# Kernel tuning notes

Hardware: AMD Instinct MI355X
Metric: run time of the kernel (lower is better)

The kernel has to match this reference:

```python
import jax, jax.numpy as jnp
import numpy as np

IN_FEA = 128
OUT_FEA = 128
ALPHA = 0.2  # LeakyReLU negative slope
NEG_INF = -1.0e12


def setup_inputs() -> dict:
    key = jax.random.key(0)
    k1, k2, k3, k4 = jax.random.split(key, 4)
    b, n = 8, 2048
    inp = jax.random.normal(k1, (b, n, IN_FEA), dtype=jnp.float32)
    adj = jax.random.randint(k2, (b, n, n), 0, 2, dtype=jnp.int32)
    # xavier_uniform with gain=1.414
    def xavier(k, shape, gain=1.414):
        fan_in, fan_out = shape[0], shape[1]
        limit = gain * np.sqrt(6.0 / (fan_in + fan_out))
        return jax.random.uniform(k, shape, jnp.float32, -limit, limit)
    W = xavier(k3, (IN_FEA, OUT_FEA))
    a = xavier(k4, (2 * OUT_FEA, 1))
    return {"inp": inp, "adj": adj, "W": W, "a": a}


def reference(inp, adj, W, a):
    # h: [b, n, d]
    h = jnp.matmul(inp, W)
    # Original builds [b, n*n, 2d] via repeat/view; equivalently split a into
    # a1 (applied to h_j, the 'chunks' half) and a2 (applied to h_i).
    d = h.shape[-1]
    a1 = a[:d, 0]   # [d]
    a2 = a[d:, 0]   # [d]
    f1 = jnp.einsum('bnd,d->bn', h, a1)  # contributes per-column (j)
    f2 = jnp.einsum('bnd,d->bn', h, a2)  # contributes per-row (i)
    e = jax.nn.leaky_relu(f2[:, :, None] + f1[:, None, :], negative_slope=ALPHA)  # [b, n, n]
    logits = jnp.where(adj > 0, e, NEG_INF)
    attention = jax.nn.softmax(logits, axis=-1)
    out_h = jnp.matmul(attention, h)
    out_h = jax.nn.elu(out_h) + h  # concat=True branch
    return out_h
```

## Files before the change

kernel.cpp:

```cpp
#include <hip/hip_runtime.h>
#include <hip/hip_bf16.h>

typedef __bf16 bf16x8 __attribute__((ext_vector_type(8)));
typedef __bf16 bf16x4 __attribute__((ext_vector_type(4)));
typedef float  f32x4  __attribute__((ext_vector_type(4)));

#define LRELU_ALPHA 0.2f
#define LOG2E 1.44269504088896340736f

__device__ __forceinline__ float fexp2(float x) {
#if __has_builtin(__builtin_amdgcn_exp2f)
    return __builtin_amdgcn_exp2f(x);
#else
    float r; asm("v_exp_f32 %0, %1" : "=v"(r) : "v"(x)); return r;
#endif
}

__device__ __forceinline__ void wg_barrier() {
    asm volatile("s_waitcnt lgkmcnt(0)" ::: "memory");
    __builtin_amdgcn_s_barrier();
    asm volatile("" ::: "memory");
}

__global__ __launch_bounds__(128) void gat_prep(
    const float* __restrict__ inp, const float* __restrict__ W,
    const float* __restrict__ a,
    __bf16* __restrict__ hb, float* __restrict__ f1, float* __restrict__ f2)
{
    const int r0 = blockIdx.x << 3;
    const int d  = threadIdx.x;
    __shared__ float sIn[8][128];
    __shared__ float sRed[8][4];
    #pragma unroll
    for (int r = 0; r < 8; ++r)
        sIn[r][d] = inp[(size_t)(r0 + r) * 128 + d];
    __syncthreads();

    float acc[8] = {0.f,0.f,0.f,0.f,0.f,0.f,0.f,0.f};
    #pragma unroll 4
    for (int k = 0; k < 128; ++k) {
        float wv = W[k * 128 + d];
        #pragma unroll
        for (int r = 0; r < 8; ++r) acc[r] += sIn[r][k] * wv;
    }

    const float a1 = a[d], a2 = a[128 + d];
    const int wv = d >> 6;
    #pragma unroll
    for (int r = 0; r < 8; ++r) {
        hb[(size_t)(r0 + r) * 128 + d] = (__bf16)acc[r];
        float t1 = acc[r] * a1;
        float t2 = acc[r] * a2;
        #pragma unroll
        for (int m = 1; m < 64; m <<= 1) {
            t1 += __shfl_xor(t1, m);
            t2 += __shfl_xor(t2, m);
        }
        if ((d & 63) == 0) { sRed[r][wv] = t1; sRed[r][2 + wv] = t2; }
    }
    __syncthreads();
    if (d < 8) {
        f1[r0 + d] = (sRed[d][0] + sRed[d][1]) * LOG2E;
        f2[r0 + d] = (sRed[d][2] + sRed[d][3]) * LOG2E;
    }
}

__global__ __launch_bounds__(256) void gat_f1max(
    const float* __restrict__ f1, float* __restrict__ f1max)
{
    const int b = blockIdx.x;
    const int t = threadIdx.x;
    float m = -1e30f;
    for (int j = t; j < 2048; j += 256) m = fmaxf(m, f1[b * 2048 + j]);
    #pragma unroll
    for (int k = 1; k < 64; k <<= 1) m = fmaxf(m, __shfl_xor(m, k));
    __shared__ float sm[4];
    if ((t & 63) == 0) sm[t >> 6] = m;
    __syncthreads();
    if (t == 0) f1max[b] = fmaxf(fmaxf(sm[0], sm[1]), fmaxf(sm[2], sm[3]));
}

__global__ __launch_bounds__(256) void gat_pack(
    const __bf16* __restrict__ hb, __bf16* __restrict__ pack)
{
    __shared__ __bf16 tile[64][72];
    const int tid = threadIdx.x;
    const int bidx = blockIdx.x;
    const int b  = bidx >> 6;
    const int tI = bidx & 63;
    const int n0 = (tI >> 1) << 6;
    const int d0 = (tI & 1) << 6;
    #pragma unroll
    for (int pass = 0; pass < 2; ++pass) {
        int row = (tid >> 3) + (pass << 5);
        int c   = (tid & 7) << 3;
        *(bf16x8*)&tile[row][c] =
            *(const bf16x8*)(hb + (size_t)(b * 2048 + n0 + row) * 128 + d0 + c);
    }
    __syncthreads();
    const int lane = tid & 63;
    const int il = lane & 15;
    const int kg = lane >> 4;
    #pragma unroll
    for (int pass = 0; pass < 2; ++pass) {
        const int f  = (tid >> 6) + (pass << 2);
        const int Dl = f >> 1;
        const int jh = f & 1;
        union { __bf16 e[8]; bf16x8 v; } u;
        #pragma unroll
        for (int e = 0; e < 8; ++e)
            u.e[e] = tile[(jh << 5) + (kg << 3) + e][(Dl << 4) + il];
        const size_t off = (((size_t)(b << 5) + (n0 >> 6)) << 13)
                         + ((size_t)((((d0 >> 4) + Dl) << 1) | jh) << 9)
                         + (lane << 3);
        *(bf16x8*)(pack + off) = u.v;
    }
}

#define PCOMPUTE(TT, BUF) do {                                                \
    const int _jb = ((TT) << 6) + (pj4 << 2);                                 \
    float4 uu = *(const float4*)&us[_jb];                                     \
    float4 vv = *(const float4*)&vs[_jb];                                     \
    float p0 = (uu.x > ti) ? ai * uu.x : bi * vv.x;                           \
    float p1 = (uu.y > ti) ? ai * uu.y : bi * vv.y;                           \
    float p2 = (uu.z > ti) ? ai * uu.z : bi * vv.z;                           \
    float p3 = (uu.w > ti) ? ai * uu.w : bi * vv.w;                           \
    p0 = (gA.x > 0) ? p0 : 0.f;                                               \
    p1 = (gA.y > 0) ? p1 : 0.f;                                               \
    p2 = (gA.z > 0) ? p2 : 0.f;                                               \
    p3 = (gA.w > 0) ? p3 : 0.f;                                               \
    bf16x4 pb;                                                                \
    pb[0] = (__bf16)p0; pb[1] = (__bf16)p1;                                   \
    pb[2] = (__bf16)p2; pb[3] = (__bf16)p3;                                   \
    den += (float)pb[0] + (float)pb[1] + (float)pb[2] + (float)pb[3];         \
    *(bf16x4*)(&Ps[BUF][pwo]) = pb;                                           \
} while (0)

__global__ __launch_bounds__(512, 4) void gat_attn11(
    const int* __restrict__ adj, const __bf16* __restrict__ hb,
    const __bf16* __restrict__ pack, const float* __restrict__ f1g,
    const float* __restrict__ f2g, const float* __restrict__ f1maxg,
    float* __restrict__ out)
{
    const int bid = ((blockIdx.x & 7) << 6) | (blockIdx.x >> 3);
    const int b  = bid >> 6;
    const int i0 = (bid & 63) << 5;
    const int tid = threadIdx.x;

    __shared__ float us[2048];
    __shared__ float vs[2048];
    __shared__ alignas(16) __bf16 Ps[2][2048];
    __shared__ float lsum[32];

    {
        float4 fv = *(const float4*)&f1g[(b << 11) + (tid << 2)];
        float4 uu, vv;
        uu.x = fexp2(fv.x); uu.y = fexp2(fv.y);
        uu.z = fexp2(fv.z); uu.w = fexp2(fv.w);
        vv.x = fexp2(LRELU_ALPHA * fv.x); vv.y = fexp2(LRELU_ALPHA * fv.y);
        vv.z = fexp2(LRELU_ALPHA * fv.z); vv.w = fexp2(LRELU_ALPHA * fv.w);
        *(float4*)&us[tid << 2] = uu;
        *(float4*)&vs[tid << 2] = vv;
    }

    const int pi  = tid >> 4;
    const int pj4 = tid & 15;
    const float fm  = f1maxg[b];
    const float f2v = f2g[(b << 11) + i0 + pi];
    const float z   = f2v + fm;
    const float M   = fmaxf(z, LRELU_ALPHA * z);
    const float ai  = fexp2(f2v - M);
    const float bi  = fexp2(__builtin_fmaf(LRELU_ALPHA, f2v, -M));
    const float ti  = fexp2(-f2v);
    const int* ajp = adj + (((size_t)(b << 11) + i0 + pi) << 11) + (pj4 << 2);
    const int pwo = (pi << 6) + ((((pj4 << 3)) ^ ((pi & 7) << 4)) >> 1);

    const int w    = tid >> 6;
    const int lane = tid & 63;
    const int il   = lane & 15;
    const int kg   = lane >> 4;
    const int ig   = w & 1;
    const int dq   = w >> 1;
    const int ai2  = (ig << 4) + il;
    const int aof0 = (ai2 << 6) + (((kg << 4) ^ ((ai2 & 7) << 4)) >> 1);
    const int aof1 = (ai2 << 6) + (((64 | (kg << 4)) ^ ((ai2 & 7) << 4)) >> 1);
    const __bf16* pB = pack + (((size_t)b << 5) << 13) + (dq << 11) + (lane << 3);

    f32x4 acc0 = {0.f,0.f,0.f,0.f}, acc1 = {0.f,0.f,0.f,0.f};
    float den = 0.f;

    int4 gA  = *(const int4*)ajp;
    int4 gA2 = *(const int4*)(ajp + 64);
    bf16x8 Bc0 = *(const bf16x8*)(pB);
    bf16x8 Bc1 = *(const bf16x8*)(pB + 512);
    bf16x8 Bc2 = *(const bf16x8*)(pB + 1024);
    bf16x8 Bc3 = *(const bf16x8*)(pB + 1536);

    wg_barrier();

    PCOMPUTE(0, 0);
    gA = gA2;
    gA2 = *(const int4*)(ajp + 128);

    wg_barrier();

    for (int t = 0; t < 31; ++t) {
        const __bf16* pBn = pB + ((size_t)(t + 1) << 13);
        bf16x8 Bn0 = *(const bf16x8*)(pBn);
        bf16x8 Bn1 = *(const bf16x8*)(pBn + 512);
        bf16x8 Bn2 = *(const bf16x8*)(pBn + 1024);
        bf16x8 Bn3 = *(const bf16x8*)(pBn + 1536);

        bf16x8 A0 = *(const bf16x8*)(&Ps[t & 1][aof0]);
        bf16x8 A1 = *(const bf16x8*)(&Ps[t & 1][aof1]);

        PCOMPUTE(t + 1, (t + 1) & 1);
        gA = gA2;
        gA2 = *(const int4*)(ajp + (((t + 3) & 31) << 6));

        acc0 = __builtin_amdgcn_mfma_f32_16x16x32_bf16(A0, Bc0, acc0, 0, 0, 0);
        acc0 = __builtin_amdgcn_mfma_f32_16x16x32_bf16(A1, Bc1, acc0, 0, 0, 0);
        acc1 = __builtin_amdgcn_mfma_f32_16x16x32_bf16(A0, Bc2, acc1, 0, 0, 0);
        acc1 = __builtin_amdgcn_mfma_f32_16x16x32_bf16(A1, Bc3, acc1, 0, 0, 0);

        Bc0 = Bn0; Bc1 = Bn1; Bc2 = Bn2; Bc3 = Bn3;

        wg_barrier();
    }

    {
        bf16x8 A0 = *(const bf16x8*)(&Ps[1][aof0]);
        bf16x8 A1 = *(const bf16x8*)(&Ps[1][aof1]);
        acc0 = __builtin_amdgcn_mfma_f32_16x16x32_bf16(A0, Bc0, acc0, 0, 0, 0);
        acc0 = __builtin_amdgcn_mfma_f32_16x16x32_bf16(A1, Bc1, acc0, 0, 0, 0);
        acc1 = __builtin_amdgcn_mfma_f32_16x16x32_bf16(A0, Bc2, acc1, 0, 0, 0);
        acc1 = __builtin_amdgcn_mfma_f32_16x16x32_bf16(A1, Bc3, acc1, 0, 0, 0);
    }

    den += __shfl_xor(den, 1);
    den += __shfl_xor(den, 2);
    den += __shfl_xor(den, 4);
    den += __shfl_xor(den, 8);
    if (pj4 == 0) lsum[pi] = den;
    wg_barrier();

    #pragma unroll
    for (int r = 0; r < 4; ++r) {
        const int   row = (kg << 2) + r;
        const float dn  = lsum[(ig << 4) + row];
        const size_t gbase = (((size_t)(b << 11) + i0 + (ig << 4) + row) << 7)
                             + (dq << 5) + il;
        float v, e;
        v = acc0[r] / dn; e = (v > 0.f) ? v : (__expf(v) - 1.f);
        out[gbase] = e + (float)hb[gbase];
        v = acc1[r] / dn; e = (v > 0.f) ? v : (__expf(v) - 1.f);
        out[gbase + 16] = e + (float)hb[gbase + 16];
    }
}

extern "C" void kernel_launch(void* const* d_in, const int* in_sizes, int n_in,
                              void* d_out, int out_size, void* d_ws, size_t ws_size,
                              hipStream_t stream)
{
    const float* inp = (const float*)d_in[0];
    const int*   adj = (const int*)d_in[1];
    const float* W   = (const float*)d_in[2];
    const float* a   = (const float*)d_in[3];
    float* out = (float*)d_out;

    char* ws = (char*)d_ws;
    __bf16* hb    = (__bf16*)ws;
    __bf16* pack  = (__bf16*)(ws + (4 << 20));
    float*  f1    = (float*)(ws + (8 << 20));
    float*  f2    = (float*)(ws + (8 << 20) + 65536);
    float*  f1max = (float*)(ws + (8 << 20) + 131072);

    gat_prep<<<2048, 128, 0, stream>>>(inp, W, a, hb, f1, f2);
    gat_f1max<<<8, 256, 0, stream>>>(f1, f1max);
    gat_pack<<<512, 256, 0, stream>>>(hb, pack);
    gat_attn11<<<512, 512, 0, stream>>>(adj, hb, pack, f1, f2, f1max, out);
}
```

Measured before the change: 58.68 us.

## Restructure attention kernel to 16-row tiles with MFMA-computed softmax denominators

```diff
diff --git a/kernel.cpp b/kernel.cpp
--- a/kernel.cpp
+++ b/kernel.cpp
@@ -2,7 +2,6 @@
 #include <hip/hip_bf16.h>
 
 typedef __bf16 bf16x8 __attribute__((ext_vector_type(8)));
-typedef __bf16 bf16x4 __attribute__((ext_vector_type(4)));
 typedef float  f32x4  __attribute__((ext_vector_type(4)));
 
 #define LRELU_ALPHA 0.2f
@@ -117,143 +116,159 @@
     }
 }
 
-#define PCOMPUTE(TT, BUF) do {                                                \
-    const int _jb = ((TT) << 6) + (pj4 << 2);                                 \
-    float4 uu = *(const float4*)&us[_jb];                                     \
-    float4 vv = *(const float4*)&vs[_jb];                                     \
-    float p0 = (uu.x > ti) ? ai * uu.x : bi * vv.x;                           \
-    float p1 = (uu.y > ti) ? ai * uu.y : bi * vv.y;                           \
-    float p2 = (uu.z > ti) ? ai * uu.z : bi * vv.z;                           \
-    float p3 = (uu.w > ti) ? ai * uu.w : bi * vv.w;                           \
-    p0 = (gA.x > 0) ? p0 : 0.f;                                               \
-    p1 = (gA.y > 0) ? p1 : 0.f;                                               \
-    p2 = (gA.z > 0) ? p2 : 0.f;                                               \
-    p3 = (gA.w > 0) ? p3 : 0.f;                                               \
-    bf16x4 pb;                                                                \
-    pb[0] = (__bf16)p0; pb[1] = (__bf16)p1;                                   \
-    pb[2] = (__bf16)p2; pb[3] = (__bf16)p3;                                   \
-    den += (float)pb[0] + (float)pb[1] + (float)pb[2] + (float)pb[3];         \
-    *(bf16x4*)(&Ps[BUF][pwo]) = pb;                                           \
-} while (0)
-
-__global__ __launch_bounds__(512, 4) void gat_attn11(
+__global__ __launch_bounds__(256, 4) void gat_attn12(
     const int* __restrict__ adj, const __bf16* __restrict__ hb,
     const __bf16* __restrict__ pack, const float* __restrict__ f1g,
     const float* __restrict__ f2g, const float* __restrict__ f1maxg,
     float* __restrict__ out)
 {
-    const int bid = ((blockIdx.x & 7) << 6) | (blockIdx.x >> 3);
-    const int b  = bid >> 6;
-    const int i0 = (bid & 63) << 5;
+    const int bid = ((blockIdx.x & 7) << 7) | (blockIdx.x >> 3);
+    const int b  = bid >> 7;
+    const int i0 = (bid & 127) << 4;
     const int tid = threadIdx.x;
 
     __shared__ float us[2048];
     __shared__ float vs[2048];
-    __shared__ alignas(16) __bf16 Ps[2][2048];
-    __shared__ float lsum[32];
-
-    {
-        float4 fv = *(const float4*)&f1g[(b << 11) + (tid << 2)];
-        float4 uu, vv;
-        uu.x = fexp2(fv.x); uu.y = fexp2(fv.y);
-        uu.z = fexp2(fv.z); uu.w = fexp2(fv.w);
-        vv.x = fexp2(LRELU_ALPHA * fv.x); vv.y = fexp2(LRELU_ALPHA * fv.y);
-        vv.z = fexp2(LRELU_ALPHA * fv.z); vv.w = fexp2(LRELU_ALPHA * fv.w);
-        *(float4*)&us[tid << 2] = uu;
-        *(float4*)&vs[tid << 2] = vv;
-    }
+    __shared__ alignas(16) __bf16 Ps[2][16 * 136];
+    __shared__ float lsum[16];
 
     const int pi  = tid >> 4;
     const int pj4 = tid & 15;
+
+    const int* ajp  = adj + (((size_t)(b << 11) + i0 + pi) << 11) + (pj4 << 3);
+    const int* ajp8 = ajp + 1024;
+
     const float fm  = f1maxg[b];
     const float f2v = f2g[(b << 11) + i0 + pi];
-    const float z   = f2v + fm;
-    const float M   = fmaxf(z, LRELU_ALPHA * z);
-    const float ai  = fexp2(f2v - M);
-    const float bi  = fexp2(__builtin_fmaf(LRELU_ALPHA, f2v, -M));
-    const float ti  = fexp2(-f2v);
-    const int* ajp = adj + (((size_t)(b << 11) + i0 + pi) << 11) + (pj4 << 2);
-    const int pwo = (pi << 6) + ((((pj4 << 3)) ^ ((pi & 7) << 4)) >> 1);
+    const float zM  = f2v + fm;
+    const float M   = fmaxf(zM, LRELU_ALPHA * zM);
+    const float ai_ = fexp2(f2v - M);
+    const float bi_ = fexp2(__builtin_fmaf(LRELU_ALPHA, f2v, -M));
+
+    int4 As[3][2];
+    As[0][0] = *(const int4*)(ajp);        As[0][1] = *(const int4*)(ajp + 4);
+    As[1][0] = *(const int4*)(ajp + 128);  As[1][1] = *(const int4*)(ajp + 132);
+    As[2][0] = *(const int4*)(ajp + 256);  As[2][1] = *(const int4*)(ajp + 260);
+
+    {
+        const int jb = tid << 3;
+        float4 f0 = *(const float4*)&f1g[(b << 11) + jb];
+        float4 f1v = *(const float4*)&f1g[(b << 11) + jb + 4];
+        float4 uu0, uu1, vv0, vv1;
+        uu0.x = fexp2(f0.x);  uu0.y = fexp2(f0.y);
+        uu0.z = fexp2(f0.z);  uu0.w = fexp2(f0.w);
+        uu1.x = fexp2(f1v.x); uu1.y = fexp2(f1v.y);
+        uu1.z = fexp2(f1v.z); uu1.w = fexp2(f1v.w);
+        vv0.x = fexp2(LRELU_ALPHA * f0.x);  vv0.y = fexp2(LRELU_ALPHA * f0.y);
+        vv0.z = fexp2(LRELU_ALPHA * f0.z);  vv0.w = fexp2(LRELU_ALPHA * f0.w);
+        vv1.x = fexp2(LRELU_ALPHA * f1v.x); vv1.y = fexp2(LRELU_ALPHA * f1v.y);
+        vv1.z = fexp2(LRELU_ALPHA * f1v.z); vv1.w = fexp2(LRELU_ALPHA * f1v.w);
+        *(float4*)&us[jb]     = uu0;  *(float4*)&us[jb + 4] = uu1;
+        *(float4*)&vs[jb]     = vv0;  *(float4*)&vs[jb + 4] = vv1;
+    }
 
     const int w    = tid >> 6;
     const int lane = tid & 63;
     const int il   = lane & 15;
     const int kg   = lane >> 4;
-    const int ig   = w & 1;
-    const int dq   = w >> 1;
-    const int ai2  = (ig << 4) + il;
-    const int aof0 = (ai2 << 6) + (((kg << 4) ^ ((ai2 & 7) << 4)) >> 1);
-    const int aof1 = (ai2 << 6) + (((64 | (kg << 4)) ^ ((ai2 & 7) << 4)) >> 1);
-    const __bf16* pB = pack + (((size_t)b << 5) << 13) + (dq << 11) + (lane << 3);
-
-    f32x4 acc0 = {0.f,0.f,0.f,0.f}, acc1 = {0.f,0.f,0.f,0.f};
-    float den = 0.f;
-
-    int4 gA  = *(const int4*)ajp;
-    int4 gA2 = *(const int4*)(ajp + 64);
-    bf16x8 Bc0 = *(const bf16x8*)(pB);
-    bf16x8 Bc1 = *(const bf16x8*)(pB + 512);
-    bf16x8 Bc2 = *(const bf16x8*)(pB + 1024);
-    bf16x8 Bc3 = *(const bf16x8*)(pB + 1536);
+    const int dq   = w;
+
+    f32x4 acc0 = {0,0,0,0}, acc1 = {0,0,0,0}, accd = {0,0,0,0};
+    union { __bf16 e[8]; bf16x8 v; } ones;
+    #pragma unroll
+    for (int x = 0; x < 8; ++x) ones.e[x] = (__bf16)1.0f;
+    const bf16x8 onesv = ones.v;
+
+#define PCOMP(TT, BUF) do {                                                   \
+    const int _jb = ((TT) << 7) + (pj4 << 3);                                 \
+    float4 _u0 = *(const float4*)&us[_jb];                                    \
+    float4 _u1 = *(const float4*)&us[_jb + 4];                                \
+    float4 _v0 = *(const float4*)&vs[_jb];                                    \
+    float4 _v1 = *(const float4*)&vs[_jb + 4];                                \
+    int4 _aA = As[(TT) % 3][0];                                               \
+    int4 _aB = As[(TT) % 3][1];                                               \
+    union { __bf16 e[8]; bf16x8 v; } _pb;                                     \
+    _pb.e[0] = (__bf16)((_aA.x > 0) ? fmaxf(ai_ * _u0.x, bi_ * _v0.x) : 0.f); \
+    _pb.e[1] = (__bf16)((_aA.y > 0) ? fmaxf(ai_ * _u0.y, bi_ * _v0.y) : 0.f); \
+    _pb.e[2] = (__bf16)((_aA.z > 0) ? fmaxf(ai_ * _u0.z, bi_ * _v0.z) : 0.f); \
+    _pb.e[3] = (__bf16)((_aA.w > 0) ? fmaxf(ai_ * _u0.w, bi_ * _v0.w) : 0.f); \
+    _pb.e[4] = (__bf16)((_aB.x > 0) ? fmaxf(ai_ * _u1.x, bi_ * _v1.x) : 0.f); \
+    _pb.e[5] = (__bf16)((_aB.y > 0) ? fmaxf(ai_ * _u1.y, bi_ * _v1.y) : 0.f); \
+    _pb.e[6] = (__bf16)((_aB.z > 0) ? fmaxf(ai_ * _u1.z, bi_ * _v1.z) : 0.f); \
+    _pb.e[7] = (__bf16)((_aB.w > 0) ? fmaxf(ai_ * _u1.w, bi_ * _v1.w) : 0.f); \
+    *(bf16x8*)&Ps[BUF][pi * 136 + (pj4 << 3)] = _pb.v;                        \
+    if ((TT) + 3 < 16) {        \
+        if ((TT) + 3 < 8) {                                                   \
+            As[(TT) % 3][0] = *(const int4*)(ajp + (((TT) + 3) << 7));        \
+            As[(TT) % 3][1] = *(const int4*)(ajp + (((TT) + 3) << 7) + 4);    \
+        } else {                                                              \
+            As[(TT) % 3][0] = *(const int4*)(ajp8 + (((TT) - 5) << 7));       \
+            As[(TT) % 3][1] = *(const int4*)(ajp8 + (((TT) - 5) << 7) + 4);   \
+        }                                                                     \
+    }                                                                         \
+} while (0)
 
     wg_barrier();
-
-    PCOMPUTE(0, 0);
-    gA = gA2;
-    gA2 = *(const int4*)(ajp + 128);
-
+    PCOMP(0, 0);
     wg_barrier();
 
-    for (int t = 0; t < 31; ++t) {
-        const __bf16* pBn = pB + ((size_t)(t + 1) << 13);
-        bf16x8 Bn0 = *(const bf16x8*)(pBn);
-        bf16x8 Bn1 = *(const bf16x8*)(pBn + 512);
-        bf16x8 Bn2 = *(const bf16x8*)(pBn + 1024);
-        bf16x8 Bn3 = *(const bf16x8*)(pBn + 1536);
-
-        bf16x8 A0 = *(const bf16x8*)(&Ps[t & 1][aof0]);
-        bf16x8 A1 = *(const bf16x8*)(&Ps[t & 1][aof1]);
-
-        PCOMPUTE(t + 1, (t + 1) & 1);
-        gA = gA2;
-        gA2 = *(const int4*)(ajp + (((t + 3) & 31) << 6));
-
-        acc0 = __builtin_amdgcn_mfma_f32_16x16x32_bf16(A0, Bc0, acc0, 0, 0, 0);
-        acc0 = __builtin_amdgcn_mfma_f32_16x16x32_bf16(A1, Bc1, acc0, 0, 0, 0);
-        acc1 = __builtin_amdgcn_mfma_f32_16x16x32_bf16(A0, Bc2, acc1, 0, 0, 0);
-        acc1 = __builtin_amdgcn_mfma_f32_16x16x32_bf16(A1, Bc3, acc1, 0, 0, 0);
-
-        Bc0 = Bn0; Bc1 = Bn1; Bc2 = Bn2; Bc3 = Bn3;
+    #pragma unroll
+    for (int t = 0; t < 16; ++t) {
+        const __bf16* bp0 = pack + (((size_t)(b << 5) + (t << 1)) << 13)
+                          + (dq << 11) + (lane << 3);
+        const __bf16* bp1 = bp0 + 8192;
+        bf16x8 B00 = *(const bf16x8*)(bp0);
+        bf16x8 B01 = *(const bf16x8*)(bp0 + 512);
+        bf16x8 B02 = *(const bf16x8*)(bp0 + 1024);
+        bf16x8 B03 = *(const bf16x8*)(bp0 + 1536);
+        bf16x8 B10 = *(const bf16x8*)(bp1);
+        bf16x8 B11 = *(const bf16x8*)(bp1 + 512);
+        bf16x8 B12 = *(const bf16x8*)(bp1 + 1024);
+        bf16x8 B13 = *(const bf16x8*)(bp1 + 1536);
+
+        if (t < 15) PCOMP(t + 1, (t + 1) & 1);
+
+        const __bf16* pr = &Ps[t & 1][0];
+        const int abase = il * 136 + kg * 8;
+        bf16x8 Af0 = *(const bf16x8*)(pr + abase);
+        bf16x8 Af1 = *(const bf16x8*)(pr + abase + 32);
+        bf16x8 Af2 = *(const bf16x8*)(pr + abase + 64);
+        bf16x8 Af3 = *(const bf16x8*)(pr + abase + 96);
+
+        acc0 = __builtin_amdgcn_mfma_f32_16x16x32_bf16(Af0, B00, acc0, 0,0,0);
+        acc1 = __builtin_amdgcn_mfma_f32_16x16x32_bf16(Af0, B02, acc1, 0,0,0);
+        acc0 = __builtin_amdgcn_mfma_f32_16x16x32_bf16(Af1, B01, acc0, 0,0,0);
+        acc1 = __builtin_amdgcn_mfma_f32_16x16x32_bf16(Af1, B03, acc1, 0,0,0);
+        acc0 = __builtin_amdgcn_mfma_f32_16x16x32_bf16(Af2, B10, acc0, 0,0,0);
+        acc1 = __builtin_amdgcn_mfma_f32_16x16x32_bf16(Af2, B12, acc1, 0,0,0);
+        acc0 = __builtin_amdgcn_mfma_f32_16x16x32_bf16(Af3, B11, acc0, 0,0,0);
+        acc1 = __builtin_amdgcn_mfma_f32_16x16x32_bf16(Af3, B13, acc1, 0,0,0);
+        if (dq == 0) {
+            accd = __builtin_amdgcn_mfma_f32_16x16x32_bf16(Af0, onesv, accd, 0,0,0);
+            accd = __builtin_amdgcn_mfma_f32_16x16x32_bf16(Af1, onesv, accd, 0,0,0);
+            accd = __builtin_amdgcn_mfma_f32_16x16x32_bf16(Af2, onesv, accd, 0,0,0);
+            accd = __builtin_amdgcn_mfma_f32_16x16x32_bf16(Af3, onesv, accd, 0,0,0);
+        }
 
         wg_barrier();
     }
-
-    {
-        bf16x8 A0 = *(const bf16x8*)(&Ps[1][aof0]);
-        bf16x8 A1 = *(const bf16x8*)(&Ps[1][aof1]);
-        acc0 = __builtin_amdgcn_mfma_f32_16x16x32_bf16(A0, Bc0, acc0, 0, 0, 0);
-        acc0 = __builtin_amdgcn_mfma_f32_16x16x32_bf16(A1, Bc1, acc0, 0, 0, 0);
-        acc1 = __builtin_amdgcn_mfma_f32_16x16x32_bf16(A0, Bc2, acc1, 0, 0, 0);
-        acc1 = __builtin_amdgcn_mfma_f32_16x16x32_bf16(A1, Bc3, acc1, 0, 0, 0);
-    }
-
-    den += __shfl_xor(den, 1);
-    den += __shfl_xor(den, 2);
-    den += __shfl_xor(den, 4);
-    den += __shfl_xor(den, 8);
-    if (pj4 == 0) lsum[pi] = den;
+#undef PCOMP
+
+    if (dq == 0 && il == 0) {
+        #pragma unroll
+        for (int r = 0; r < 4; ++r) lsum[(kg << 2) + r] = accd[r];
+    }
     wg_barrier();
 
     #pragma unroll
     for (int r = 0; r < 4; ++r) {
-        const int   row = (kg << 2) + r;
-        const float dn  = lsum[(ig << 4) + row];
-        const size_t gbase = (((size_t)(b << 11) + i0 + (ig << 4) + row) << 7)
-                             + (dq << 5) + il;
+        const int   row  = (kg << 2) + r;
+        const float rden = 1.0f / lsum[row];
+        const size_t gbase = (((size_t)(b << 11) + i0 + row) << 7) + (dq << 5) + il;
         float v, e;
-        v = acc0[r] / dn; e = (v > 0.f) ? v : (__expf(v) - 1.f);
+        v = acc0[r] * rden; e = (v > 0.f) ? v : (fexp2(v * LOG2E) - 1.f);
         out[gbase] = e + (float)hb[gbase];
-        v = acc1[r] / dn; e = (v > 0.f) ? v : (__expf(v) - 1.f);
+        v = acc1[r] * rden; e = (v > 0.f) ? v : (fexp2(v * LOG2E) - 1.f);
         out[gbase + 16] = e + (float)hb[gbase + 16];
     }
 }
@@ -278,5 +293,5 @@
     gat_prep<<<2048, 128, 0, stream>>>(inp, W, a, hb, f1, f2);
     gat_f1max<<<8, 256, 0, stream>>>(f1, f1max);
     gat_pack<<<512, 256, 0, stream>>>(hb, pack);
-    gat_attn11<<<512, 512, 0, stream>>>(adj, hb, pack, f1, f2, f1max, out);
-}
+    gat_attn12<<<1024, 256, 0, stream>>>(adj, hb, pack, f1, f2, f1max, out);
+}
```

New measurement: 64.42 us. 9.8% more time.
